# Optimization experiments

Measured on AMD Instinct MI355X. Metric: run time of the kernel, lower is better.

Reference implementation:

```python
import jax, jax.numpy as jnp
import numpy as np

E = 512      # embed_dim
H = 8        # num_heads
D = E // H   # head_dim = 64
R = 32       # rot_dims (partial rotary)
THETA = 10000.0


def _rope(x):
    # x: [B, H, S, D]; rotate first R dims (interleaved pairs, lucidrains-style)
    S = x.shape[-2]
    inv_freq = THETA ** (-jnp.arange(0, R, 2, dtype=jnp.float32) / R)  # [R/2]
    ang = jnp.arange(S, dtype=jnp.float32)[:, None] * inv_freq          # [S, R/2]
    c, s = jnp.cos(ang), jnp.sin(ang)
    xr, xp = x[..., :R], x[..., R:]
    x1, x2 = xr[..., 0::2], xr[..., 1::2]
    rot = jnp.stack([x1 * c - x2 * s, x1 * s + x2 * c], axis=-1).reshape(xr.shape)
    return jnp.concatenate([rot, xp], axis=-1)


def setup_inputs() -> dict:
    key = jax.random.key(0)
    k1, k2, k3, k4 = jax.random.split(key, 4)
    B, S = 4, 2048
    x = jax.random.normal(k1, (B, S, E), dtype=jnp.float32)
    input_mask = jax.random.randint(k2, (B, S), 0, 2).astype(bool)
    W_in = jax.random.normal(k3, (3 * E, E), dtype=jnp.float32) / np.sqrt(E).astype(np.float32)
    W_out = jax.random.normal(k4, (E, E), dtype=jnp.float32) / np.sqrt(E).astype(np.float32)
    return {"x": x, "input_mask": input_mask, "W_in": W_in, "W_out": W_out}


def reference(x, input_mask, W_in, W_out):
    B, S, _ = x.shape
    # fused QKV projection (Linear, no bias): x @ W_in.T -> [B,S,3E]
    qkv = (x @ W_in.T).reshape(B, S, 3, H, D).transpose(2, 0, 3, 1, 4)  # [3,B,H,S,D]
    q, k, v = qkv[0], qkv[1], qkv[2]
    q = _rope(q)
    k = _rope(k)
    # mask: causal AND (both tokens valid OR diagonal)
    causal = jnp.tril(jnp.ones((S, S), dtype=bool))
    inv = ~input_mask                                  # [B,S]
    cross = inv[:, None, :] | inv[:, :, None]          # [B,S,S]
    square = (~cross) | jnp.eye(S, dtype=bool)         # diagonal forced True
    full = causal[None, :, :] & square                 # [B,S,S]
    scores = jnp.einsum('bhsd,bhtd->bhst', q, k) / np.float32(np.sqrt(D))
    scores = jnp.where(full[:, None, :, :], scores, -jnp.inf)
    probs = jax.nn.softmax(scores, axis=-1)
    attn = jnp.einsum('bhst,bhtd->bhsd', probs, v)
    attn = attn.transpose(0, 2, 1, 3).reshape(B, S, E)
    return attn @ W_out.T
```

## Files before the change

kernel.cpp:

```cpp
#include <hip/hip_runtime.h>
#include <math.h>

#define B_ 4
#define S_ 2048
#define E_ 512
#define H_ 8
#define D_ 64

typedef short bf16x8 __attribute__((ext_vector_type(8)));
typedef float f32x4 __attribute__((ext_vector_type(4)));

__device__ inline short f2bf(float f) {
  union { float f; unsigned u; } v; v.f = f;
  unsigned r = v.u + 0x7FFF + ((v.u >> 16) & 1);
  return (short)(r >> 16);
}
__device__ inline short f2bf_fast(float f) {
  union { float f; unsigned u; } v; v.f = f;
  return (short)((v.u + 0x8000u) >> 16);
}

__global__ __launch_bounds__(256) void cvt_bf16(const float* __restrict__ src,
                                                short* __restrict__ dst, int n4) {
  int i = blockIdx.x * 256 + threadIdx.x;
  if (i < n4) {
    float4 f = ((const float4*)src)[i];
    short4 o;
    o.x = f2bf(f.x); o.y = f2bf(f.y); o.z = f2bf(f.z); o.w = f2bf(f.w);
    ((short4*)dst)[i] = o;
  }
}

__global__ __launch_bounds__(256) void gemm_qkv_mfma(
    const short* __restrict__ Xb,
    const short* __restrict__ Wb,
    short* __restrict__ qb, short* __restrict__ kb, short* __restrict__ vbT) {
  __shared__ __align__(16) short As[128][40];
  __shared__ __align__(16) short Bs[128][40];
  const int tid = threadIdx.x;
  const int w = tid >> 6, lane = tid & 63;
  const int l15 = lane & 15, quad = lane >> 4;
  const int wm = w & 1, wn = w >> 1;
  const int m0 = blockIdx.x * 128;
  const int n0 = blockIdx.y * 128;
  f32x4 acc[4][4];
  for (int mt = 0; mt < 4; ++mt)
    for (int nt = 0; nt < 4; ++nt) acc[mt][nt] = (f32x4){0.f, 0.f, 0.f, 0.f};

  for (int k0 = 0; k0 < E_; k0 += 32) {
    __syncthreads();
    for (int l = 0; l < 2; ++l) {
      int c = tid + 256 * l;
      int row = c >> 2, k8 = (c & 3) * 8;
      *(bf16x8*)&As[row][k8] = *(const bf16x8*)&Xb[(size_t)(m0 + row) * E_ + k0 + k8];
      *(bf16x8*)&Bs[row][k8] = *(const bf16x8*)&Wb[(size_t)(n0 + row) * E_ + k0 + k8];
    }
    __syncthreads();
    bf16x8 a[4], bfr[4];
    for (int mt = 0; mt < 4; ++mt)
      a[mt] = *(const bf16x8*)&As[wm * 64 + mt * 16 + l15][quad * 8];
    for (int nt = 0; nt < 4; ++nt)
      bfr[nt] = *(const bf16x8*)&Bs[wn * 64 + nt * 16 + l15][quad * 8];
    for (int mt = 0; mt < 4; ++mt)
      for (int nt = 0; nt < 4; ++nt)
        acc[mt][nt] = __builtin_amdgcn_mfma_f32_16x16x32_bf16(a[mt], bfr[nt], acc[mt][nt], 0, 0, 0);
  }
  const int t3 = n0 >> 9;
  for (int nt = 0; nt < 4; ++nt) {
    const int n = n0 + wn * 64 + nt * 16 + l15;
    const int h = (n >> 6) & 7;
    const int d = n & 63;
    const bool dorope = (t3 < 2) && (d < 32);
    const float sgn = (d & 1) ? 1.f : -1.f;
    const float fr = dorope ? powf(10000.f, -(float)(2 * (d >> 1)) * (1.f / 32.f)) : 0.f;
    for (int mt = 0; mt < 4; ++mt) {
      for (int i = 0; i < 4; ++i) {
        const int m = m0 + wm * 64 + mt * 16 + quad * 4 + i;
        const int b = m >> 11, s = m & (S_ - 1);
        float val = acc[mt][nt][i];
        float pv = __shfl_xor(val, 1, 64);
        float outv = val;
        if (dorope) {
          float ang = (float)s * fr;
          float sn, cs;
          sincosf(ang, &sn, &cs);
          outv = val * cs + pv * sgn * sn;
        }
        if (t3 == 2)
          vbT[((size_t)(b * 8 + h) * D_ + d) * S_ + s] = f2bf(outv);
        else {
          short* dst = (t3 == 0) ? qb : kb;
          dst[(((size_t)(b * 8 + h)) * S_ + s) * D_ + d] = f2bf(outv);
        }
      }
    }
  }
}

__global__ __launch_bounds__(256) void gemm_out_mfma(
    const short* __restrict__ Ab, const short* __restrict__ Wb,
    float* __restrict__ out) {
  __shared__ __align__(16) short As[128][40];
  __shared__ __align__(16) short Bs[128][40];
  const int tid = threadIdx.x;
  const int w = tid >> 6, lane = tid & 63;
  const int l15 = lane & 15, quad = lane >> 4;
  const int wm = w & 1, wn = w >> 1;
  const int m0 = blockIdx.x * 128;
  const int n0 = blockIdx.y * 128;
  f32x4 acc[4][4];
  for (int mt = 0; mt < 4; ++mt)
    for (int nt = 0; nt < 4; ++nt) acc[mt][nt] = (f32x4){0.f, 0.f, 0.f, 0.f};

  for (int k0 = 0; k0 < E_; k0 += 32) {
    __syncthreads();
    for (int l = 0; l < 2; ++l) {
      int c = tid + 256 * l;
      int row = c >> 2, k8 = (c & 3) * 8;
      *(bf16x8*)&As[row][k8] = *(const bf16x8*)&Ab[(size_t)(m0 + row) * E_ + k0 + k8];
      *(bf16x8*)&Bs[row][k8] = *(const bf16x8*)&Wb[(size_t)(n0 + row) * E_ + k0 + k8];
    }
    __syncthreads();
    bf16x8 a[4], bfr[4];
    for (int mt = 0; mt < 4; ++mt)
      a[mt] = *(const bf16x8*)&As[wm * 64 + mt * 16 + l15][quad * 8];
    for (int nt = 0; nt < 4; ++nt)
      bfr[nt] = *(const bf16x8*)&Bs[wn * 64 + nt * 16 + l15][quad * 8];
    for (int mt = 0; mt < 4; ++mt)
      for (int nt = 0; nt < 4; ++nt)
        acc[mt][nt] = __builtin_amdgcn_mfma_f32_16x16x32_bf16(a[mt], bfr[nt], acc[mt][nt], 0, 0, 0);
  }
  for (int mt = 0; mt < 4; ++mt)
    for (int nt = 0; nt < 4; ++nt) {
      const int n = n0 + wn * 64 + nt * 16 + l15;
      for (int i = 0; i < 4; ++i) {
        const int m = m0 + wm * 64 + mt * 16 + quad * 4 + i;
        out[(size_t)m * E_ + n] = acc[mt][nt][i];
      }
    }
}

__global__ __launch_bounds__(256) void flash_mfma(
    const short* __restrict__ qb, const short* __restrict__ kb,
    const short* __restrict__ vbT, const int* __restrict__ maskp,
    short* __restrict__ ob) {
  __shared__ __align__(16) short Ks[64][72];
  __shared__ __align__(16) short VT[64][72];
  __shared__ __align__(16) short Pl[4][16][72];
  __shared__ float kbias[64];
  const int tid = threadIdx.x;
  const int w = tid >> 6, lane = tid & 63;
  const int l15 = lane & 15, quad = lane >> 4;
  const int bid = blockIdx.x;
  const int u = bid & 7, v = bid >> 3;
  const int bh = (u << 2) | (v & 3);
  const int pair = v >> 2;
  const int b = bh >> 3, h = bh & 7;
  const short* qbase = qb + (size_t)bh * S_ * D_;
  const short* kbase = kb + (size_t)bh * S_ * D_;
  const short* vtb   = vbT + (size_t)bh * D_ * S_;
  const float c2 = 0.1803368801f;
  bf16x8 ones;
  for (int j = 0; j < 8; ++j) ones[j] = (short)0x3F80;

  for (int seg = 0; seg < 2; ++seg) {
    const int qt = (seg == 0) ? pair : 31 - pair;
    const int r0 = qt * 64;
    bf16x8 aq[2];
    {
      const short* qrow = qbase + (size_t)(r0 + 16 * w + l15) * D_;
      aq[0] = *(const bf16x8*)&qrow[quad * 8];
      aq[1] = *(const bf16x8*)&qrow[32 + quad * 8];
    }
    f32x4 o[4], lsum;
    for (int no = 0; no < 4; ++no) o[no] = (f32x4){0.f, 0.f, 0.f, 0.f};
    lsum = (f32x4){0.f, 0.f, 0.f, 0.f};

    for (int kt = 0; kt <= qt; ++kt) {
      const int t0 = kt * 64;
      __syncthreads();
      for (int l = 0; l < 2; ++l) {
        int idx = tid + 256 * l;
        int row = idx >> 3, ch = (idx & 7) * 8;
        *(bf16x8*)&Ks[row][ch] = *(const bf16x8*)(kbase + (size_t)(t0 + row) * D_ + ch);
        *(bf16x8*)&VT[row][ch] = *(const bf16x8*)(vtb + (size_t)row * S_ + t0 + ch);
      }
      if (tid < 64)
        kbias[tid] = maskp[b * S_ + t0 + tid] ? -23.08312f : -1.0e38f;
      __syncthreads();
      f32x4 sfr[4];
      for (int nb = 0; nb < 4; ++nb) sfr[nb] = (f32x4){0.f, 0.f, 0.f, 0.f};
      for (int nb = 0; nb < 4; ++nb)
        for (int ks = 0; ks < 2; ++ks) {
          bf16x8 bk = *(const bf16x8*)&Ks[l15 + 16 * nb][32 * ks + quad * 8];
          sfr[nb] = __builtin_amdgcn_mfma_f32_16x16x32_bf16(aq[ks], bk, sfr[nb], 0, 0, 0);
        }
      if (kt < qt) {
        for (int nb = 0; nb < 4; ++nb) {
          const float bb = kbias[l15 + 16 * nb];
          for (int i = 0; i < 4; ++i)
            Pl[w][quad * 4 + i][l15 + 16 * nb] = f2bf_fast(exp2f(sfr[nb][i] * c2 + bb));
        }
      } else {
        for (int nb = 0; nb < 4; ++nb) {
          const int tg = l15 + 16 * nb;
          const float bb = kbias[l15 + 16 * nb];
          for (int i = 0; i < 4; ++i) {
            const float bbi = (tg > 16 * w + quad * 4 + i) ? -1.0e38f : bb;
            Pl[w][quad * 4 + i][l15 + 16 * nb] = f2bf_fast(exp2f(sfr[nb][i] * c2 + bbi));
          }
        }
      }
      asm volatile("s_waitcnt lgkmcnt(0)" ::: "memory");
      bf16x8 ap0 = *(const bf16x8*)&Pl[w][l15][quad * 8];
      bf16x8 ap1 = *(const bf16x8*)&Pl[w][l15][32 + quad * 8];
      for (int no = 0; no < 4; ++no) {
        bf16x8 bv0 = *(const bf16x8*)&VT[16 * no + l15][quad * 8];
        bf16x8 bv1 = *(const bf16x8*)&VT[16 * no + l15][32 + quad * 8];
        o[no] = __builtin_amdgcn_mfma_f32_16x16x32_bf16(ap0, bv0, o[no], 0, 0, 0);
        o[no] = __builtin_amdgcn_mfma_f32_16x16x32_bf16(ap1, bv1, o[no], 0, 0, 0);
      }
      lsum = __builtin_amdgcn_mfma_f32_16x16x32_bf16(ap0, ones, lsum, 0, 0, 0);
      lsum = __builtin_amdgcn_mfma_f32_16x16x32_bf16(ap1, ones, lsum, 0, 0, 0);
    }
    for (int i = 0; i < 4; ++i) {
      const int s = r0 + 16 * w + quad * 4 + i;
      const int qm = maskp[b * S_ + s];
      const float inv = 1.f / lsum[i];
      short* orow = ob + ((size_t)(b * S_ + s)) * E_ + h * D_;
      for (int no = 0; no < 4; ++no) {
        const int d = l15 + 16 * no;
        orow[d] = qm ? f2bf(o[no][i] * inv) : vtb[(size_t)d * S_ + s];
      }
    }
  }
}

extern "C" void kernel_launch(void* const* d_in, const int* in_sizes, int n_in,
                              void* d_out, int out_size, void* d_ws, size_t ws_size,
                              hipStream_t stream) {
  const float* x    = (const float*)d_in[0];
  const int*   mask = (const int*)d_in[1];
  const float* Win  = (const float*)d_in[2];
  const float* Wout = (const float*)d_in[3];
  float* out = (float*)d_out;

  short* Xb    = (short*)d_ws;
  short* Winb  = Xb + 8192 * 512;
  short* Woutb = Winb + 1536 * 512;
  short* qb    = Woutb + 512 * 512;
  short* kb    = qb + 32 * 2048 * 64;
  short* vbT   = kb + 32 * 2048 * 64;
  short* ob    = vbT + 32 * 2048 * 64;

  cvt_bf16<<<4096, 256, 0, stream>>>(x, Xb, 8192 * 512 / 4);
  cvt_bf16<<<768, 256, 0, stream>>>(Win, Winb, 1536 * 512 / 4);
  cvt_bf16<<<256, 256, 0, stream>>>(Wout, Woutb, 512 * 512 / 4);
  gemm_qkv_mfma<<<dim3(64, 12), 256, 0, stream>>>(Xb, Winb, qb, kb, vbT);
  flash_mfma<<<512, 256, 0, stream>>>(qb, kb, vbT, mask, ob);
  gemm_out_mfma<<<dim3(64, 4), 256, 0, stream>>>(ob, Woutb, out);
}
```

Baseline: 191.1 us.

## Double-buffer K/V tiles in flash attention with register prefetch

Splits the K, V^T and key-bias shared-memory tiles into two buffers. The next tile is loaded into registers at the start of each iteration, then written to the alternate buffer after the PV MFMAs. This cuts each iteration from two barriers to one and hides global-load latency behind the QK^T and softmax compute. In exchange it doubles the LDS footprint for K/V and raises register pressure, which may lower occupancy.

```diff
diff --git a/kernel.cpp b/kernel.cpp
--- a/kernel.cpp
+++ b/kernel.cpp
@@ -144,10 +144,10 @@
     const short* __restrict__ qb, const short* __restrict__ kb,
     const short* __restrict__ vbT, const int* __restrict__ maskp,
     short* __restrict__ ob) {
-  __shared__ __align__(16) short Ks[64][72];
-  __shared__ __align__(16) short VT[64][72];
+  __shared__ __align__(16) short Ks[2][64][72];
+  __shared__ __align__(16) short VT[2][64][72];
   __shared__ __align__(16) short Pl[4][16][72];
-  __shared__ float kbias[64];
+  __shared__ float kbias[2][64];
   const int tid = threadIdx.x;
   const int w = tid >> 6, lane = tid & 63;
   const int l15 = lane & 15, quad = lane >> 4;
@@ -160,6 +160,7 @@
   const short* kbase = kb + (size_t)bh * S_ * D_;
   const short* vtb   = vbT + (size_t)bh * D_ * S_;
   const float c2 = 0.1803368801f;
+  const int srow = tid >> 3, sch = (tid & 7) * 8;
   bf16x8 ones;
   for (int j = 0; j < 8; ++j) ones[j] = (short)0x3F80;
 
@@ -176,35 +177,49 @@
     for (int no = 0; no < 4; ++no) o[no] = (f32x4){0.f, 0.f, 0.f, 0.f};
     lsum = (f32x4){0.f, 0.f, 0.f, 0.f};
 
+    {
+      bf16x8 kv0 = *(const bf16x8*)(kbase + (size_t)srow * D_ + sch);
+      bf16x8 kv1 = *(const bf16x8*)(kbase + (size_t)(32 + srow) * D_ + sch);
+      bf16x8 vv0 = *(const bf16x8*)(vtb + (size_t)srow * S_ + sch);
+      bf16x8 vv1 = *(const bf16x8*)(vtb + (size_t)(32 + srow) * S_ + sch);
+      int km = (tid < 64) ? maskp[b * S_ + tid] : 0;
+      __syncthreads();
+      *(bf16x8*)&Ks[0][srow][sch] = kv0;
+      *(bf16x8*)&Ks[0][32 + srow][sch] = kv1;
+      *(bf16x8*)&VT[0][srow][sch] = vv0;
+      *(bf16x8*)&VT[0][32 + srow][sch] = vv1;
+      if (tid < 64) kbias[0][tid] = km ? -23.08312f : -1.0e38f;
+      __syncthreads();
+    }
+
     for (int kt = 0; kt <= qt; ++kt) {
-      const int t0 = kt * 64;
-      __syncthreads();
-      for (int l = 0; l < 2; ++l) {
-        int idx = tid + 256 * l;
-        int row = idx >> 3, ch = (idx & 7) * 8;
-        *(bf16x8*)&Ks[row][ch] = *(const bf16x8*)(kbase + (size_t)(t0 + row) * D_ + ch);
-        *(bf16x8*)&VT[row][ch] = *(const bf16x8*)(vtb + (size_t)row * S_ + t0 + ch);
-      }
-      if (tid < 64)
-        kbias[tid] = maskp[b * S_ + t0 + tid] ? -23.08312f : -1.0e38f;
-      __syncthreads();
+      const int cur = kt & 1;
+      bf16x8 kv0, kv1, vv0, vv1; int km = 0;
+      if (kt < qt) {
+        const int t1 = (kt + 1) * 64;
+        kv0 = *(const bf16x8*)(kbase + (size_t)(t1 + srow) * D_ + sch);
+        kv1 = *(const bf16x8*)(kbase + (size_t)(t1 + 32 + srow) * D_ + sch);
+        vv0 = *(const bf16x8*)(vtb + (size_t)srow * S_ + t1 + sch);
+        vv1 = *(const bf16x8*)(vtb + (size_t)(32 + srow) * S_ + t1 + sch);
+        km = (tid < 64) ? maskp[b * S_ + t1 + tid] : 0;
+      }
       f32x4 sfr[4];
       for (int nb = 0; nb < 4; ++nb) sfr[nb] = (f32x4){0.f, 0.f, 0.f, 0.f};
       for (int nb = 0; nb < 4; ++nb)
         for (int ks = 0; ks < 2; ++ks) {
-          bf16x8 bk = *(const bf16x8*)&Ks[l15 + 16 * nb][32 * ks + quad * 8];
+          bf16x8 bk = *(const bf16x8*)&Ks[cur][l15 + 16 * nb][32 * ks + quad * 8];
           sfr[nb] = __builtin_amdgcn_mfma_f32_16x16x32_bf16(aq[ks], bk, sfr[nb], 0, 0, 0);
         }
       if (kt < qt) {
         for (int nb = 0; nb < 4; ++nb) {
-          const float bb = kbias[l15 + 16 * nb];
+          const float bb = kbias[cur][l15 + 16 * nb];
           for (int i = 0; i < 4; ++i)
             Pl[w][quad * 4 + i][l15 + 16 * nb] = f2bf_fast(exp2f(sfr[nb][i] * c2 + bb));
         }
       } else {
         for (int nb = 0; nb < 4; ++nb) {
           const int tg = l15 + 16 * nb;
-          const float bb = kbias[l15 + 16 * nb];
+          const float bb = kbias[cur][l15 + 16 * nb];
           for (int i = 0; i < 4; ++i) {
             const float bbi = (tg > 16 * w + quad * 4 + i) ? -1.0e38f : bb;
             Pl[w][quad * 4 + i][l15 + 16 * nb] = f2bf_fast(exp2f(sfr[nb][i] * c2 + bbi));
@@ -215,13 +230,22 @@
       bf16x8 ap0 = *(const bf16x8*)&Pl[w][l15][quad * 8];
       bf16x8 ap1 = *(const bf16x8*)&Pl[w][l15][32 + quad * 8];
       for (int no = 0; no < 4; ++no) {
-        bf16x8 bv0 = *(const bf16x8*)&VT[16 * no + l15][quad * 8];
-        bf16x8 bv1 = *(const bf16x8*)&VT[16 * no + l15][32 + quad * 8];
+        bf16x8 bv0 = *(const bf16x8*)&VT[cur][16 * no + l15][quad * 8];
+        bf16x8 bv1 = *(const bf16x8*)&VT[cur][16 * no + l15][32 + quad * 8];
         o[no] = __builtin_amdgcn_mfma_f32_16x16x32_bf16(ap0, bv0, o[no], 0, 0, 0);
         o[no] = __builtin_amdgcn_mfma_f32_16x16x32_bf16(ap1, bv1, o[no], 0, 0, 0);
       }
       lsum = __builtin_amdgcn_mfma_f32_16x16x32_bf16(ap0, ones, lsum, 0, 0, 0);
       lsum = __builtin_amdgcn_mfma_f32_16x16x32_bf16(ap1, ones, lsum, 0, 0, 0);
+      if (kt < qt) {
+        const int nxt = cur ^ 1;
+        *(bf16x8*)&Ks[nxt][srow][sch] = kv0;
+        *(bf16x8*)&Ks[nxt][32 + srow][sch] = kv1;
+        *(bf16x8*)&VT[nxt][srow][sch] = vv0;
+        *(bf16x8*)&VT[nxt][32 + srow][sch] = vv1;
+        if (tid < 64) kbias[nxt][tid] = km ? -23.08312f : -1.0e38f;
+      }
+      __syncthreads();
     }
     for (int i = 0; i < 4; ++i) {
       const int s = r0 + 16 * w + quad * 4 + i;
```

New measurement: 187.6 us. About the same (-1.8%).

## Split attention KV range across two blocks and merge partial outputs

Applied to the files above, without the earlier changes.

The attention kernel now launches twice as many blocks. Each block handles half of the causal key tiles for a query tile and writes an unnormalized partial output and row sum to scratch buffers. A new merge kernel adds the two partials and normalizes them. This doubles parallelism on a 512-block launch, which underfills the GPU, at the cost of extra global traffic, an extra launch, and partials rounded to bf16 before the merge. It relies on a fixed softmax offset rather than a running max, so partials can be added without rescaling.

```diff
diff --git a/kernel.cpp b/kernel.cpp
--- a/kernel.cpp
+++ b/kernel.cpp
@@ -18,6 +18,10 @@
 __device__ inline short f2bf_fast(float f) {
   union { float f; unsigned u; } v; v.f = f;
   return (short)((v.u + 0x8000u) >> 16);
+}
+__device__ inline float bf2f(short s) {
+  union { unsigned u; float f; } v; v.u = ((unsigned)(unsigned short)s) << 16;
+  return v.f;
 }
 
 __global__ __launch_bounds__(256) void cvt_bf16(const float* __restrict__ src,
@@ -143,6 +147,8 @@
 __global__ __launch_bounds__(256) void flash_mfma(
     const short* __restrict__ qb, const short* __restrict__ kb,
     const short* __restrict__ vbT, const int* __restrict__ maskp,
+    short* __restrict__ pb0, short* __restrict__ pb1,
+    float* __restrict__ lb0, float* __restrict__ lb1,
     short* __restrict__ ob) {
   __shared__ __align__(16) short Ks[64][72];
   __shared__ __align__(16) short VT[64][72];
@@ -154,11 +160,15 @@
   const int bid = blockIdx.x;
   const int u = bid & 7, v = bid >> 3;
   const int bh = (u << 2) | (v & 3);
-  const int pair = v >> 2;
-  const int b = bh >> 3, h = bh & 7;
+  const int w2 = v >> 2;
+  const int pair = w2 & 15;
+  const int kh = w2 >> 4;
+  const int b = bh >> 3, hd = bh & 7;
   const short* qbase = qb + (size_t)bh * S_ * D_;
   const short* kbase = kb + (size_t)bh * S_ * D_;
   const short* vtb   = vbT + (size_t)bh * D_ * S_;
+  short* PB = kh ? pb1 : pb0;
+  float* LB = kh ? lb1 : lb0;
   const float c2 = 0.1803368801f;
   bf16x8 ones;
   for (int j = 0; j < 8; ++j) ones[j] = (short)0x3F80;
@@ -166,6 +176,9 @@
   for (int seg = 0; seg < 2; ++seg) {
     const int qt = (seg == 0) ? pair : 31 - pair;
     const int r0 = qt * 64;
+    const int mid = (qt + 2) >> 1;
+    const int lo = kh ? mid : 0;
+    const int hi = kh ? (qt + 1) : mid;
     bf16x8 aq[2];
     {
       const short* qrow = qbase + (size_t)(r0 + 16 * w + l15) * D_;
@@ -176,7 +189,7 @@
     for (int no = 0; no < 4; ++no) o[no] = (f32x4){0.f, 0.f, 0.f, 0.f};
     lsum = (f32x4){0.f, 0.f, 0.f, 0.f};
 
-    for (int kt = 0; kt <= qt; ++kt) {
+    for (int kt = lo; kt < hi; ++kt) {
       const int t0 = kt * 64;
       __syncthreads();
       for (int l = 0; l < 2; ++l) {
@@ -226,14 +239,38 @@
     for (int i = 0; i < 4; ++i) {
       const int s = r0 + 16 * w + quad * 4 + i;
       const int qm = maskp[b * S_ + s];
-      const float inv = 1.f / lsum[i];
-      short* orow = ob + ((size_t)(b * S_ + s)) * E_ + h * D_;
-      for (int no = 0; no < 4; ++no) {
-        const int d = l15 + 16 * no;
-        orow[d] = qm ? f2bf(o[no][i] * inv) : vtb[(size_t)d * S_ + s];
-      }
-    }
-  }
+      const size_t row = (size_t)(b * S_ + s) * E_ + hd * D_;
+      if (kh == 0 && !qm) {
+        for (int no = 0; no < 4; ++no) {
+          const int d = l15 + 16 * no;
+          ob[row + d] = vtb[(size_t)d * S_ + s];
+        }
+      }
+      for (int no = 0; no < 4; ++no)
+        PB[row + l15 + 16 * no] = f2bf(o[no][i]);
+      if (l15 == 0)
+        LB[bh * S_ + s] = lsum[i];
+    }
+  }
+}
+
+__global__ __launch_bounds__(256) void merge_kernel(
+    const short* __restrict__ pb0, const short* __restrict__ pb1,
+    const float* __restrict__ lb0, const float* __restrict__ lb1,
+    const int* __restrict__ maskp, short* __restrict__ ob) {
+  int idx = blockIdx.x * 256 + threadIdx.x;
+  int m = idx >> 6, e = (idx & 63) * 8;
+  if (!maskp[m]) return;
+  int b = m >> 11, s = m & (S_ - 1);
+  int bh = b * 8 + (e >> 6);
+  float l = lb0[bh * S_ + s] + lb1[bh * S_ + s];
+  float inv = 1.f / l;
+  bf16x8 p0 = *(const bf16x8*)&pb0[(size_t)m * E_ + e];
+  bf16x8 p1 = *(const bf16x8*)&pb1[(size_t)m * E_ + e];
+  bf16x8 r;
+  for (int j = 0; j < 8; ++j)
+    r[j] = f2bf((bf2f(p0[j]) + bf2f(p1[j])) * inv);
+  *(bf16x8*)&ob[(size_t)m * E_ + e] = r;
 }
 
 extern "C" void kernel_launch(void* const* d_in, const int* in_sizes, int n_in,
@@ -252,11 +289,16 @@
   short* kb    = qb + 32 * 2048 * 64;
   short* vbT   = kb + 32 * 2048 * 64;
   short* ob    = vbT + 32 * 2048 * 64;
+  short* pb0   = ob + 8192 * 512;
+  short* pb1   = pb0 + 8192 * 512;
+  float* lb0   = (float*)(pb1 + 8192 * 512);
+  float* lb1   = lb0 + 32 * 2048;
 
   cvt_bf16<<<4096, 256, 0, stream>>>(x, Xb, 8192 * 512 / 4);
   cvt_bf16<<<768, 256, 0, stream>>>(Win, Winb, 1536 * 512 / 4);
   cvt_bf16<<<256, 256, 0, stream>>>(Wout, Woutb, 512 * 512 / 4);
   gemm_qkv_mfma<<<dim3(64, 12), 256, 0, stream>>>(Xb, Winb, qb, kb, vbT);
-  flash_mfma<<<512, 256, 0, stream>>>(qb, kb, vbT, mask, ob);
+  flash_mfma<<<1024, 256, 0, stream>>>(qb, kb, vbT, mask, pb0, pb1, lb0, lb1, ob);
+  merge_kernel<<<2048, 256, 0, stream>>>(pb0, pb1, lb0, lb1, mask, ob);
   gemm_out_mfma<<<dim3(64, 4), 256, 0, stream>>>(ob, Woutb, out);
 }
```

After: 178.3 us. 6.7% less time.
